# Kernel tuning notes

Hardware: AMD Instinct MI355X
Metric: run time of the kernel (lower is better)

Reference implementation:

```python
import jax, jax.numpy as jnp
import numpy as np

N = 100000
C_IN = 256
C_OUT = 256
LN_EPS = 1e-5


def setup_inputs() -> dict:
    key = jax.random.key(0)
    ks = jax.random.split(key, 6)
    x = jax.random.normal(ks[0], (N, C_IN), dtype=jnp.float32)
    idx1 = jax.random.randint(ks[1], (N,), 0, N, dtype=jnp.int64 if jax.config.jax_enable_x64 else jnp.int32)
    idx2 = jax.random.randint(ks[2], (N,), 0, N, dtype=idx1.dtype)
    idx3 = jax.random.randint(ks[3], (N,), 0, N, dtype=idx1.dtype)
    idx4 = jax.random.randint(ks[4], (N,), 0, N, dtype=idx1.dtype)
    W = jax.random.normal(ks[5], (5 * C_IN, C_OUT), dtype=jnp.float32) * (1.0 / np.sqrt(5 * C_IN))
    b = jnp.zeros((C_OUT,), dtype=jnp.float32)
    gamma = jnp.ones((C_OUT,), dtype=jnp.float32)
    beta = jnp.zeros((C_OUT,), dtype=jnp.float32)
    return {"x": x, "idx1": idx1, "idx2": idx2, "idx3": idx3, "idx4": idx4,
            "W": W, "b": b, "gamma": gamma, "beta": beta}


def reference(x, idx1, idx2, idx3, idx4, W, b, gamma, beta):
    # Four sparse-mm neighbor gathers (one nonzero of value 1 per row)
    a = x[idx1]
    bb = x[idx2]
    c = x[idx3]
    d = x[idx4]
    # symmetric combine + concat -> [N, 5*C_IN]
    patch = jnp.concatenate([x, jnp.abs(a - c), a + c, jnp.abs(bb - d), bb + d], axis=-1)
    y = patch @ W + b
    # LayerNorm over channels
    mu = jnp.mean(y, axis=-1, keepdims=True)
    var = jnp.mean(jnp.square(y - mu), axis=-1, keepdims=True)
    y = (y - mu) * jax.lax.rsqrt(var + LN_EPS) * gamma + beta
    # residual (in_channels == out_channels -> identity projection)
    y = y + x
    # torch nn.GELU default is exact (erf) gelu
    return jax.nn.gelu(y, approximate=False)
```

## Files before the change

kernel.cpp:

```cpp
#include <hip/hip_runtime.h>


#define N_ROWS   100000
#define C        256
#define BK       32
#define NCHUNK   40
#define BM       64
#define CHUNK_V  1024
#define LN_EPS   1e-5f

typedef __bf16 bf16;
typedef bf16  bf16x8 __attribute__((ext_vector_type(8)));
typedef float f32x4  __attribute__((ext_vector_type(4)));

union BV  { bf16x8 v; bf16 h[8]; };
union FV2 { float4 q[2]; float f[8]; };

#define LBAR() asm volatile("s_waitcnt lgkmcnt(0)\n\ts_barrier" ::: "memory")

__global__ void wprep(const float* __restrict__ W, bf16* __restrict__ Wt) {
    int t = blockIdx.x * 256 + threadIdx.x;
    if (t >= NCHUNK * 4 * 4 * 64) return;
    int lane = t & 63;
    int ni   = (t >> 6) & 3;
    int wv   = (t >> 8) & 3;
    int kc   = t >> 10;
    int l16  = lane & 15, quad = lane >> 4;
    int n = wv * 64 + ni * 16 + l16;
    int base;
    if (kc < 8)       base = kc * 32;
    else if (kc < 24) { int u = kc - 8;  base = 256 + (u & 1) * 256 + (u >> 1) * 32; }
    else              { int u = kc - 24; base = 768 + (u & 1) * 256 + (u >> 1) * 32; }
    BV o;
    #pragma unroll
    for (int e = 0; e < 8; ++e) {
        int kRow = base + quad * 8 + e;
        o.h[e] = (bf16)W[(size_t)kRow * C + n];
    }
    ((bf16x8*)Wt)[t] = o.v;
}

__global__ __launch_bounds__(256, 3)
void fused(const float* __restrict__ x,
           const int* __restrict__ idx1, const int* __restrict__ idx2,
           const int* __restrict__ idx3, const int* __restrict__ idx4,
           const bf16* __restrict__ Wt,
           const float* __restrict__ bias,
           const float* __restrict__ gamma_, const float* __restrict__ beta_,
           float* __restrict__ out)
{
    __shared__ __align__(16) union {
        bf16 a[2][BM * BK];
        struct { float rsum[BM][4]; float rsq[BM][4]; float mu[BM]; float rs[BM]; } red;
    } SA;

    const int tid  = threadIdx.x;
    const int lane = tid & 63;
    const int wv   = tid >> 6;
    const int quad = lane >> 4;
    const int l16  = lane & 15;
    const int r0   = blockIdx.x * BM;

    const int r_st = tid >> 2;
    const int q_st = tid & 3;
    int gr_self = r0 + r_st; if (gr_self >= N_ROWS) gr_self = 0;
    const int ia = idx1[gr_self], ib = idx2[gr_self];
    const int ic = idx3[gr_self], id = idx4[gr_self];

    const int a_w_off = r_st * 32 + ((q_st ^ ((r_st >> 1) & 3)) << 3);
    int a_r_off[4];
    #pragma unroll
    for (int mi = 0; mi < 4; ++mi) {
        int m = mi * 16 + l16;
        a_r_off[mi] = m * 32 + ((quad ^ ((m >> 1) & 3)) << 3);
    }

    const bf16x8* Wq = (const bf16x8*)Wt + wv * 256 + lane;

    f32x4 acc[4][4] = {};
    bf16x8 hold;
    bf16x8 wf[4], wfn[4];

    {
        const float4* p = (const float4*)(x + (size_t)gr_self * C + (q_st << 3));
        FV2 u; u.q[0] = p[0]; u.q[1] = p[1];
        #pragma unroll
        for (int j = 0; j < 4; ++j) wf[j] = Wq[j * 64];
        BV b0;
        #pragma unroll
        for (int j = 0; j < 8; ++j) b0.h[j] = (bf16)u.f[j];
        *(bf16x8*)&SA.a[0][a_w_off] = b0.v;
    }
    LBAR();

    for (int kc = 0; kc < NCHUNK; ++kc) {
        const int kn = kc + 1;

        FV2 la, lc;
        int mode = 0;
        if (kn < 8) {
            mode = 1;
            const float4* p = (const float4*)(x + (size_t)gr_self * C + (kn << 5) + (q_st << 3));
            la.q[0] = p[0]; la.q[1] = p[1];
        } else if (kn < NCHUNK) {
            int u = (kn < 24) ? (kn - 8) : (kn - 24);
            if (!(u & 1)) {
                mode = 2;
                int rA = (kn < 24) ? ia : ib;
                int rC = (kn < 24) ? ic : id;
                int off = ((u >> 1) << 5) + (q_st << 3);
                const float4* pa = (const float4*)(x + (size_t)rA * C + off);
                const float4* pc = (const float4*)(x + (size_t)rC * C + off);
                la.q[0] = pa[0]; la.q[1] = pa[1];
                lc.q[0] = pc[0]; lc.q[1] = pc[1];
            }
        }

        if (kn < NCHUNK) {
            const bf16x8* wp = Wq + (size_t)kn * CHUNK_V;
            #pragma unroll
            for (int j = 0; j < 4; ++j) wfn[j] = wp[j * 64];
        }

        {
            const bf16* Ab = SA.a[kc & 1];
            bf16x8 af[4];
            #pragma unroll
            for (int mi = 0; mi < 4; ++mi)
                af[mi] = *(const bf16x8*)&Ab[a_r_off[mi]];
            __builtin_amdgcn_s_setprio(1);
            #pragma unroll
            for (int mi = 0; mi < 4; ++mi)
                #pragma unroll
                for (int ni = 0; ni < 4; ++ni)
                    acc[mi][ni] = __builtin_amdgcn_mfma_f32_16x16x32_bf16(
                        af[mi], wf[ni], acc[mi][ni], 0, 0, 0);
            __builtin_amdgcn_s_setprio(0);
        }

        if (kn < NCHUNK) {
            BV sv;
            if (mode == 1) {
                #pragma unroll
                for (int j = 0; j < 8; ++j) sv.h[j] = (bf16)la.f[j];
            } else if (mode == 2) {
                BV hs;
                #pragma unroll
                for (int j = 0; j < 8; ++j) {
                    sv.h[j] = (bf16)fabsf(la.f[j] - lc.f[j]);
                    hs.h[j] = (bf16)(la.f[j] + lc.f[j]);
                }
                hold = hs.v;
            } else {
                sv.v = hold;
            }
            *(bf16x8*)&SA.a[kn & 1][a_w_off] = sv.v;
            #pragma unroll
            for (int j = 0; j < 4; ++j) wf[j] = wfn[j];
            LBAR();
        }
    }

    float bcol[4], gcol[4], ecol[4];
    #pragma unroll
    for (int ni = 0; ni < 4; ++ni) {
        int cidx = wv * 64 + ni * 16 + l16;
        bcol[ni] = bias[cidx]; gcol[ni] = gamma_[cidx]; ecol[ni] = beta_[cidx];
    }
    #pragma unroll
    for (int mi = 0; mi < 4; ++mi)
        #pragma unroll
        for (int ni = 0; ni < 4; ++ni)
            #pragma unroll
            for (int rg = 0; rg < 4; ++rg)
                acc[mi][ni][rg] += bcol[ni];

    #pragma unroll
    for (int mi = 0; mi < 4; ++mi) {
        #pragma unroll
        for (int rg = 0; rg < 4; ++rg) {
            float s = 0.f, q = 0.f;
            #pragma unroll
            for (int ni = 0; ni < 4; ++ni) {
                float y = acc[mi][ni][rg];
                s += y; q += y * y;
            }
            #pragma unroll
            for (int m = 1; m <= 8; m <<= 1) {
                s += __shfl_xor(s, m, 64);
                q += __shfl_xor(q, m, 64);
            }
            if (l16 == 0) {
                int row = mi * 16 + quad * 4 + rg;
                SA.red.rsum[row][wv] = s;
                SA.red.rsq [row][wv] = q;
            }
        }
    }
    __syncthreads();
    if (tid < BM) {
        float s  = SA.red.rsum[tid][0] + SA.red.rsum[tid][1] + SA.red.rsum[tid][2] + SA.red.rsum[tid][3];
        float q  = SA.red.rsq [tid][0] + SA.red.rsq [tid][1] + SA.red.rsq [tid][2] + SA.red.rsq [tid][3];
        float mu = s * (1.0f / C);
        float var = q * (1.0f / C) - mu * mu;
        SA.red.mu[tid] = mu;
        SA.red.rs[tid] = rsqrtf(var + LN_EPS);
    }
    __syncthreads();

    #pragma unroll
    for (int mi = 0; mi < 4; ++mi) {
        #pragma unroll
        for (int rg = 0; rg < 4; ++rg) {
            int row  = mi * 16 + quad * 4 + rg;
            int grow = r0 + row;
            if (grow >= N_ROWS) continue;
            float mu = SA.red.mu[row], rs = SA.red.rs[row];
            #pragma unroll
            for (int ni = 0; ni < 4; ++ni) {
                int cidx = wv * 64 + ni * 16 + l16;
                float y = (acc[mi][ni][rg] - mu) * rs * gcol[ni] + ecol[ni];
                y += x[(size_t)grow * C + cidx];
                float g = 0.5f * y * (1.0f + erff(y * 0.70710678118654752f));
                out[(size_t)grow * C + cidx] = g;
            }
        }
    }
}

extern "C" void kernel_launch(void* const* d_in, const int* in_sizes, int n_in,
                              void* d_out, int out_size, void* d_ws, size_t ws_size,
                              hipStream_t stream) {
    const float* x  = (const float*)d_in[0];
    const int*   i1 = (const int*)d_in[1];
    const int*   i2 = (const int*)d_in[2];
    const int*   i3 = (const int*)d_in[3];
    const int*   i4 = (const int*)d_in[4];
    const float* W  = (const float*)d_in[5];
    const float* b  = (const float*)d_in[6];
    const float* gm = (const float*)d_in[7];
    const float* bt = (const float*)d_in[8];
    float* outp = (float*)d_out;
    bf16* Wt = (bf16*)d_ws;

    wprep<<<(NCHUNK * 4 * 4 * 64 + 255) / 256, 256, 0, stream>>>(W, Wt);
    fused<<<(N_ROWS + BM - 1) / BM, 256, 0, stream>>>(
        x, i1, i2, i3, i4, Wt, b, gm, bt, outp);
}
```

Measured before the change: 346.3 us.

## Prefetch gathered x rows two chunks ahead and fully unroll K loop

Global loads of x (own row and gathered neighbour rows) are now issued two K-chunks ahead and held in registers as cur/nxt buffers, so each chunk's LDS store uses data loaded an iteration earlier rather than waiting on a fresh gather. The LDS store of the next tile now comes before the MFMA block instead of after it. The 40-chunk loop is fully unrolled so the mode branches resolve at compile time. This aims to hide gather latency behind the matrix work, at the cost of extra registers (two more FV2 pairs) that may pressure occupancy at 3 blocks per CU, plus larger code.

```diff
diff --git a/kernel.cpp b/kernel.cpp
--- a/kernel.cpp
+++ b/kernel.cpp
@@ -66,6 +66,7 @@
     int gr_self = r0 + r_st; if (gr_self >= N_ROWS) gr_self = 0;
     const int ia = idx1[gr_self], ib = idx2[gr_self];
     const int ic = idx3[gr_self], id = idx4[gr_self];
+    const float* xself = x + (size_t)gr_self * C + (q_st << 3);
 
     const int a_w_off = r_st * 32 + ((q_st ^ ((r_st >> 1) & 3)) << 3);
     int a_r_off[4];
@@ -80,12 +81,18 @@
     f32x4 acc[4][4] = {};
     bf16x8 hold;
     bf16x8 wf[4], wfn[4];
+    FV2 cur_a, cur_c;
+    FV2 nxt_a, nxt_c;
+    int cur_mode, nxt_mode;
 
     {
-        const float4* p = (const float4*)(x + (size_t)gr_self * C + (q_st << 3));
-        FV2 u; u.q[0] = p[0]; u.q[1] = p[1];
+        const float4* p0 = (const float4*)xself;
+        float4 s0 = p0[0], s1 = p0[1];
+        const float4* p1 = (const float4*)(xself + 32);
+        cur_a.q[0] = p1[0]; cur_a.q[1] = p1[1]; cur_mode = 1;
         #pragma unroll
         for (int j = 0; j < 4; ++j) wf[j] = Wq[j * 64];
+        FV2 u; u.q[0] = s0; u.q[1] = s1;
         BV b0;
         #pragma unroll
         for (int j = 0; j < 8; ++j) b0.h[j] = (bf16)u.f[j];
@@ -93,26 +100,29 @@
     }
     LBAR();
 
+    #pragma unroll
     for (int kc = 0; kc < NCHUNK; ++kc) {
         const int kn = kc + 1;
-
-        FV2 la, lc;
-        int mode = 0;
-        if (kn < 8) {
-            mode = 1;
-            const float4* p = (const float4*)(x + (size_t)gr_self * C + (kn << 5) + (q_st << 3));
-            la.q[0] = p[0]; la.q[1] = p[1];
-        } else if (kn < NCHUNK) {
-            int u = (kn < 24) ? (kn - 8) : (kn - 24);
-            if (!(u & 1)) {
-                mode = 2;
-                int rA = (kn < 24) ? ia : ib;
-                int rC = (kn < 24) ? ic : id;
-                int off = ((u >> 1) << 5) + (q_st << 3);
-                const float4* pa = (const float4*)(x + (size_t)rA * C + off);
-                const float4* pc = (const float4*)(x + (size_t)rC * C + off);
-                la.q[0] = pa[0]; la.q[1] = pa[1];
-                lc.q[0] = pc[0]; lc.q[1] = pc[1];
+        const int kp = kc + 2;
+
+        nxt_mode = 0;
+        if (kp < NCHUNK) {
+            if (kp < 8) {
+                nxt_mode = 1;
+                const float4* p = (const float4*)(xself + (kp << 5));
+                nxt_a.q[0] = p[0]; nxt_a.q[1] = p[1];
+            } else {
+                int u = (kp < 24) ? (kp - 8) : (kp - 24);
+                if (!(u & 1)) {
+                    nxt_mode = 2;
+                    int rA = (kp < 24) ? ia : ib;
+                    int rC = (kp < 24) ? ic : id;
+                    int off = ((u >> 1) << 5) + (q_st << 3);
+                    const float4* pa = (const float4*)(x + (size_t)rA * C + off);
+                    const float4* pc = (const float4*)(x + (size_t)rC * C + off);
+                    nxt_a.q[0] = pa[0]; nxt_a.q[1] = pa[1];
+                    nxt_c.q[0] = pc[0]; nxt_c.q[1] = pc[1];
+                }
             }
         }
 
@@ -120,6 +130,25 @@
             const bf16x8* wp = Wq + (size_t)kn * CHUNK_V;
             #pragma unroll
             for (int j = 0; j < 4; ++j) wfn[j] = wp[j * 64];
+        }
+
+        if (kn < NCHUNK) {
+            BV sv;
+            if (cur_mode == 1) {
+                #pragma unroll
+                for (int j = 0; j < 8; ++j) sv.h[j] = (bf16)cur_a.f[j];
+            } else if (cur_mode == 2) {
+                BV hs;
+                #pragma unroll
+                for (int j = 0; j < 8; ++j) {
+                    sv.h[j] = (bf16)fabsf(cur_a.f[j] - cur_c.f[j]);
+                    hs.h[j] = (bf16)(cur_a.f[j] + cur_c.f[j]);
+                }
+                hold = hs.v;
+            } else {
+                sv.v = hold;
+            }
+            *(bf16x8*)&SA.a[kn & 1][a_w_off] = sv.v;
         }
 
         {
@@ -139,26 +168,12 @@
         }
 
         if (kn < NCHUNK) {
-            BV sv;
-            if (mode == 1) {
-                #pragma unroll
-                for (int j = 0; j < 8; ++j) sv.h[j] = (bf16)la.f[j];
-            } else if (mode == 2) {
-                BV hs;
-                #pragma unroll
-                for (int j = 0; j < 8; ++j) {
-                    sv.h[j] = (bf16)fabsf(la.f[j] - lc.f[j]);
-                    hs.h[j] = (bf16)(la.f[j] + lc.f[j]);
-                }
-                hold = hs.v;
-            } else {
-                sv.v = hold;
-            }
-            *(bf16x8*)&SA.a[kn & 1][a_w_off] = sv.v;
             #pragma unroll
             for (int j = 0; j < 4; ++j) wf[j] = wfn[j];
-            LBAR();
-        }
+        }
+        cur_a = nxt_a; cur_c = nxt_c; cur_mode = nxt_mode;
+
+        if (kn < NCHUNK) LBAR();
     }
 
     float bcol[4], gcol[4], ecol[4];
```

Result: faster. 334.3 us (-3.4%).

## Give each wave its own 16 rows and all 256 columns, dropping shared memory

Applied to the files above, without the earlier changes.

The work split changes from four waves sharing 64 rows through double-buffered LDS A tiles to each wave owning 16 rows across all 256 output columns. The A operand is built directly in registers from prefetched x and gather loads, which removes every LDS write, read and barrier in the K loop. LayerNorm statistics are now reduced inside a wave with shuffles instead of through shared memory. The cost is that each wave now streams the full bf16 weight matrix with per-iteration global loads instead of one quarter of it, raising L2 traffic and register pressure (16 accumulators plus 8 weight fragments) under a three-block occupancy target.

```diff
diff --git a/kernel.cpp b/kernel.cpp
--- a/kernel.cpp
+++ b/kernel.cpp
@@ -6,7 +6,6 @@
 #define BK       32
 #define NCHUNK   40
 #define BM       64
-#define CHUNK_V  1024
 #define LN_EPS   1e-5f
 
 typedef __bf16 bf16;
@@ -16,17 +15,14 @@
 union BV  { bf16x8 v; bf16 h[8]; };
 union FV2 { float4 q[2]; float f[8]; };
 
-#define LBAR() asm volatile("s_waitcnt lgkmcnt(0)\n\ts_barrier" ::: "memory")
-
 __global__ void wprep(const float* __restrict__ W, bf16* __restrict__ Wt) {
     int t = blockIdx.x * 256 + threadIdx.x;
-    if (t >= NCHUNK * 4 * 4 * 64) return;
+    if (t >= NCHUNK * 16 * 64) return;
     int lane = t & 63;
-    int ni   = (t >> 6) & 3;
-    int wv   = (t >> 8) & 3;
+    int f    = (t >> 6) & 15;
     int kc   = t >> 10;
     int l16  = lane & 15, quad = lane >> 4;
-    int n = wv * 64 + ni * 16 + l16;
+    int n = ((f >> 2) << 6) + ((f & 3) << 4) + l16;
     int base;
     if (kc < 8)       base = kc * 32;
     else if (kc < 24) { int u = kc - 8;  base = 256 + (u & 1) * 256 + (u >> 1) * 32; }
@@ -39,6 +35,13 @@
     }
     ((bf16x8*)Wt)[t] = o.v;
 }
+
+#define ISSUE_PAIR(P) do {                                                            \
+    const float* _ba = x + (size_t)((P) < 8 ? ia : ib) * C + (((P) & 7) << 5) + (quad << 3); \
+    const float* _bc = x + (size_t)((P) < 8 ? ic : id) * C + (((P) & 7) << 5) + (quad << 3); \
+    pal.q[0] = ((const float4*)_ba)[0]; pal.q[1] = ((const float4*)_ba)[1];           \
+    pcl.q[0] = ((const float4*)_bc)[0]; pcl.q[1] = ((const float4*)_bc)[1];           \
+} while (0)
 
 __global__ __launch_bounds__(256, 3)
 void fused(const float* __restrict__ x,
@@ -49,11 +52,6 @@
            const float* __restrict__ gamma_, const float* __restrict__ beta_,
            float* __restrict__ out)
 {
-    __shared__ __align__(16) union {
-        bf16 a[2][BM * BK];
-        struct { float rsum[BM][4]; float rsq[BM][4]; float mu[BM]; float rs[BM]; } red;
-    } SA;
-
     const int tid  = threadIdx.x;
     const int lane = tid & 63;
     const int wv   = tid >> 6;
@@ -61,169 +59,130 @@
     const int l16  = lane & 15;
     const int r0   = blockIdx.x * BM;
 
-    const int r_st = tid >> 2;
-    const int q_st = tid & 3;
-    int gr_self = r0 + r_st; if (gr_self >= N_ROWS) gr_self = 0;
-    const int ia = idx1[gr_self], ib = idx2[gr_self];
-    const int ic = idx3[gr_self], id = idx4[gr_self];
-
-    const int a_w_off = r_st * 32 + ((q_st ^ ((r_st >> 1) & 3)) << 3);
-    int a_r_off[4];
-    #pragma unroll
-    for (int mi = 0; mi < 4; ++mi) {
-        int m = mi * 16 + l16;
-        a_r_off[mi] = m * 32 + ((quad ^ ((m >> 1) & 3)) << 3);
-    }
-
-    const bf16x8* Wq = (const bf16x8*)Wt + wv * 256 + lane;
-
-    f32x4 acc[4][4] = {};
-    bf16x8 hold;
-    bf16x8 wf[4], wfn[4];
+    int r_ld = r0 + wv * 16 + l16; if (r_ld >= N_ROWS) r_ld = 0;
+    const int ia = idx1[r_ld], ib = idx2[r_ld];
+    const int ic = idx3[r_ld], id = idx4[r_ld];
+    const float* xrow = x + (size_t)r_ld * C + (quad << 3);
+
+    const bf16x8* Wq = (const bf16x8*)Wt + lane;
+
+    f32x4 acc[16] = {};
+    bf16x8 wf[8];
+    bf16x8 af, af_hold;
+    FV2 s0l, s1l;
+    FV2 pal, pcl;
 
     {
-        const float4* p = (const float4*)(x + (size_t)gr_self * C + (q_st << 3));
-        FV2 u; u.q[0] = p[0]; u.q[1] = p[1];
-        #pragma unroll
-        for (int j = 0; j < 4; ++j) wf[j] = Wq[j * 64];
-        BV b0;
-        #pragma unroll
-        for (int j = 0; j < 8; ++j) b0.h[j] = (bf16)u.f[j];
-        *(bf16x8*)&SA.a[0][a_w_off] = b0.v;
-    }
-    LBAR();
-
+        const float4* p0 = (const float4*)xrow;
+        s0l.q[0] = p0[0]; s0l.q[1] = p0[1];
+        const float4* p1 = (const float4*)(xrow + 32);
+        s1l.q[0] = p1[0]; s1l.q[1] = p1[1];
+    }
+
+    #pragma unroll
     for (int kc = 0; kc < NCHUNK; ++kc) {
-        const int kn = kc + 1;
-
-        FV2 la, lc;
-        int mode = 0;
-        if (kn < 8) {
-            mode = 1;
-            const float4* p = (const float4*)(x + (size_t)gr_self * C + (kn << 5) + (q_st << 3));
-            la.q[0] = p[0]; la.q[1] = p[1];
-        } else if (kn < NCHUNK) {
-            int u = (kn < 24) ? (kn - 8) : (kn - 24);
-            if (!(u & 1)) {
-                mode = 2;
-                int rA = (kn < 24) ? ia : ib;
-                int rC = (kn < 24) ? ic : id;
-                int off = ((u >> 1) << 5) + (q_st << 3);
-                const float4* pa = (const float4*)(x + (size_t)rA * C + off);
-                const float4* pc = (const float4*)(x + (size_t)rC * C + off);
-                la.q[0] = pa[0]; la.q[1] = pa[1];
-                lc.q[0] = pc[0]; lc.q[1] = pc[1];
+        #pragma unroll
+        for (int f = 0; f < 8; ++f) wf[f] = Wq[(kc * 16 + f) * 64];
+
+        if (kc < 8) {
+            BV t;
+            if (kc & 1) {
+                #pragma unroll
+                for (int j = 0; j < 8; ++j) t.h[j] = (bf16)s1l.f[j];
+            } else {
+                #pragma unroll
+                for (int j = 0; j < 8; ++j) t.h[j] = (bf16)s0l.f[j];
             }
-        }
-
-        if (kn < NCHUNK) {
-            const bf16x8* wp = Wq + (size_t)kn * CHUNK_V;
+            af = t.v;
+            if (kc < 6) {
+                const float4* p = (const float4*)(xrow + ((kc + 2) << 5));
+                if (kc & 1) { s1l.q[0] = p[0]; s1l.q[1] = p[1]; }
+                else        { s0l.q[0] = p[0]; s0l.q[1] = p[1]; }
+            } else if (kc == 6) {
+                ISSUE_PAIR(0);
+            }
+        } else if (!((kc - 8) & 1)) {
+            const int p = (kc < 24) ? ((kc - 8) >> 1) : (((kc - 24) >> 1) + 8);
+            BV d, s;
             #pragma unroll
-            for (int j = 0; j < 4; ++j) wfn[j] = wp[j * 64];
-        }
-
-        {
-            const bf16* Ab = SA.a[kc & 1];
-            bf16x8 af[4];
-            #pragma unroll
-            for (int mi = 0; mi < 4; ++mi)
-                af[mi] = *(const bf16x8*)&Ab[a_r_off[mi]];
-            __builtin_amdgcn_s_setprio(1);
-            #pragma unroll
-            for (int mi = 0; mi < 4; ++mi)
-                #pragma unroll
-                for (int ni = 0; ni < 4; ++ni)
-                    acc[mi][ni] = __builtin_amdgcn_mfma_f32_16x16x32_bf16(
-                        af[mi], wf[ni], acc[mi][ni], 0, 0, 0);
-            __builtin_amdgcn_s_setprio(0);
-        }
-
-        if (kn < NCHUNK) {
-            BV sv;
-            if (mode == 1) {
-                #pragma unroll
-                for (int j = 0; j < 8; ++j) sv.h[j] = (bf16)la.f[j];
-            } else if (mode == 2) {
-                BV hs;
-                #pragma unroll
-                for (int j = 0; j < 8; ++j) {
-                    sv.h[j] = (bf16)fabsf(la.f[j] - lc.f[j]);
-                    hs.h[j] = (bf16)(la.f[j] + lc.f[j]);
-                }
-                hold = hs.v;
-            } else {
-                sv.v = hold;
+            for (int j = 0; j < 8; ++j) {
+                d.h[j] = (bf16)fabsf(pal.f[j] - pcl.f[j]);
+                s.h[j] = (bf16)(pal.f[j] + pcl.f[j]);
             }
-            *(bf16x8*)&SA.a[kn & 1][a_w_off] = sv.v;
-            #pragma unroll
-            for (int j = 0; j < 4; ++j) wf[j] = wfn[j];
-            LBAR();
-        }
-    }
-
-    float bcol[4], gcol[4], ecol[4];
-    #pragma unroll
-    for (int ni = 0; ni < 4; ++ni) {
-        int cidx = wv * 64 + ni * 16 + l16;
-        bcol[ni] = bias[cidx]; gcol[ni] = gamma_[cidx]; ecol[ni] = beta_[cidx];
-    }
-    #pragma unroll
-    for (int mi = 0; mi < 4; ++mi)
-        #pragma unroll
-        for (int ni = 0; ni < 4; ++ni)
-            #pragma unroll
-            for (int rg = 0; rg < 4; ++rg)
-                acc[mi][ni][rg] += bcol[ni];
-
-    #pragma unroll
-    for (int mi = 0; mi < 4; ++mi) {
-        #pragma unroll
-        for (int rg = 0; rg < 4; ++rg) {
-            float s = 0.f, q = 0.f;
-            #pragma unroll
-            for (int ni = 0; ni < 4; ++ni) {
-                float y = acc[mi][ni][rg];
-                s += y; q += y * y;
-            }
-            #pragma unroll
-            for (int m = 1; m <= 8; m <<= 1) {
-                s += __shfl_xor(s, m, 64);
-                q += __shfl_xor(q, m, 64);
-            }
-            if (l16 == 0) {
-                int row = mi * 16 + quad * 4 + rg;
-                SA.red.rsum[row][wv] = s;
-                SA.red.rsq [row][wv] = q;
-            }
-        }
-    }
-    __syncthreads();
-    if (tid < BM) {
-        float s  = SA.red.rsum[tid][0] + SA.red.rsum[tid][1] + SA.red.rsum[tid][2] + SA.red.rsum[tid][3];
-        float q  = SA.red.rsq [tid][0] + SA.red.rsq [tid][1] + SA.red.rsq [tid][2] + SA.red.rsq [tid][3];
-        float mu = s * (1.0f / C);
-        float var = q * (1.0f / C) - mu * mu;
-        SA.red.mu[tid] = mu;
-        SA.red.rs[tid] = rsqrtf(var + LN_EPS);
-    }
-    __syncthreads();
-
-    #pragma unroll
-    for (int mi = 0; mi < 4; ++mi) {
-        #pragma unroll
-        for (int rg = 0; rg < 4; ++rg) {
-            int row  = mi * 16 + quad * 4 + rg;
-            int grow = r0 + row;
-            if (grow >= N_ROWS) continue;
-            float mu = SA.red.mu[row], rs = SA.red.rs[row];
-            #pragma unroll
-            for (int ni = 0; ni < 4; ++ni) {
-                int cidx = wv * 64 + ni * 16 + l16;
-                float y = (acc[mi][ni][rg] - mu) * rs * gcol[ni] + ecol[ni];
-                y += x[(size_t)grow * C + cidx];
-                float g = 0.5f * y * (1.0f + erff(y * 0.70710678118654752f));
-                out[(size_t)grow * C + cidx] = g;
-            }
+            af = d.v; af_hold = s.v;
+            if (p < 15) ISSUE_PAIR(p + 1);
+        } else {
+            af = af_hold;
+        }
+
+        __builtin_amdgcn_s_setprio(1);
+        #pragma unroll
+        for (int f = 0; f < 8; ++f)
+            acc[f] = __builtin_amdgcn_mfma_f32_16x16x32_bf16(af, wf[f], acc[f], 0, 0, 0);
+        __builtin_amdgcn_s_setprio(0);
+
+        #pragma unroll
+        for (int f = 0; f < 8; ++f) wf[f] = Wq[(kc * 16 + 8 + f) * 64];
+
+        __builtin_amdgcn_s_setprio(1);
+        #pragma unroll
+        for (int f = 0; f < 8; ++f)
+            acc[8 + f] = __builtin_amdgcn_mfma_f32_16x16x32_bf16(af, wf[f], acc[8 + f], 0, 0, 0);
+        __builtin_amdgcn_s_setprio(0);
+    }
+
+    float bc[16];
+    #pragma unroll
+    for (int f = 0; f < 16; ++f) {
+        int cidx = ((f >> 2) << 6) + ((f & 3) << 4) + l16;
+        bc[f] = bias[cidx];
+    }
+    #pragma unroll
+    for (int f = 0; f < 16; ++f)
+        #pragma unroll
+        for (int rg = 0; rg < 4; ++rg)
+            acc[f][rg] += bc[f];
+
+    float mu[4], rs[4];
+    #pragma unroll
+    for (int rg = 0; rg < 4; ++rg) {
+        float s = 0.f, q = 0.f;
+        #pragma unroll
+        for (int f = 0; f < 16; ++f) {
+            float y = acc[f][rg];
+            s += y; q += y * y;
+        }
+        #pragma unroll
+        for (int m = 1; m <= 8; m <<= 1) {
+            s += __shfl_xor(s, m, 64);
+            q += __shfl_xor(q, m, 64);
+        }
+        float m_  = s * (1.0f / C);
+        float var = q * (1.0f / C) - m_ * m_;
+        mu[rg] = m_;
+        rs[rg] = rsqrtf(var + LN_EPS);
+    }
+
+    float gc[16], ec[16];
+    #pragma unroll
+    for (int f = 0; f < 16; ++f) {
+        int cidx = ((f >> 2) << 6) + ((f & 3) << 4) + l16;
+        gc[f] = gamma_[cidx]; ec[f] = beta_[cidx];
+    }
+
+    #pragma unroll
+    for (int rg = 0; rg < 4; ++rg) {
+        int grow = r0 + wv * 16 + quad * 4 + rg;
+        if (grow >= N_ROWS) continue;
+        const float* xr = x   + (size_t)grow * C;
+        float*       orw = out + (size_t)grow * C;
+        #pragma unroll
+        for (int f = 0; f < 16; ++f) {
+            int cidx = ((f >> 2) << 6) + ((f & 3) << 4) + l16;
+            float y = (acc[f][rg] - mu[rg]) * rs[rg] * gc[f] + ec[f];
+            y += xr[cidx];
+            float g = 0.5f * y * (1.0f + erff(y * 0.70710678118654752f));
+            orw[cidx] = g;
         }
     }
 }
@@ -243,7 +202,7 @@
     float* outp = (float*)d_out;
     bf16* Wt = (bf16*)d_ws;
 
-    wprep<<<(NCHUNK * 4 * 4 * 64 + 255) / 256, 256, 0, stream>>>(W, Wt);
+    wprep<<<(NCHUNK * 16 * 64 + 255) / 256, 256, 0, stream>>>(W, Wt);
     fused<<<(N_ROWS + BM - 1) / BM, 256, 0, stream>>>(
         x, i1, i2, i3, i4, Wt, b, gm, bt, outp);
 }
```

Result: slower. 433.9 us (+25.3%).
